# Performance work log

Hardware: AMD Instinct MI355X
Metric: run time of the kernel (lower is better)

The kernel has to match this reference:

```python
import jax, jax.numpy as jnp
import numpy as np

N, D = 8192, 128
TEMPERATURE = 0.07
EPS = 1e-8
NEG_FILL = -9e15


def setup_inputs() -> dict:
    key = jax.random.key(0)
    feats = jax.random.normal(key, (N, D), dtype=jnp.float32)
    # SimCLR-style positive-pair mask: row i's positive is row (i + N//2) % N.
    # Exactly one positive per row, as required by the original broadcast.
    label = jnp.roll(jnp.eye(N, dtype=jnp.int32), N // 2, axis=1)
    return {"feats": feats, "label": label}


def reference(feats, label):
    # F.cosine_similarity clamps each norm at eps before dividing.
    norms = jnp.linalg.norm(feats, axis=-1, keepdims=True)
    nf = feats / jnp.maximum(norms, EPS)            # [N, D] unit rows
    cos_sim = nf @ nf.T                             # [N, N] cosine similarities
    n = cos_sim.shape[0]
    self_mask = jnp.eye(n, dtype=bool)
    cos_sim = jnp.where(self_mask, NEG_FILL, cos_sim)
    cos_sim = cos_sim / TEMPERATURE
    pos_mask = (label == 1)
    # Exactly one positive per row -> masked sum == cos_sim[pos_mask] in row order.
    pos = jnp.sum(jnp.where(pos_mask, cos_sim, 0.0), axis=-1)  # [N]
    lse = jax.nn.logsumexp(cos_sim, axis=-1)                    # [N]
    return jnp.mean(-pos + lse)
```

## Files before the change

kernel.cpp:

```cpp
#include <hip/hip_runtime.h>


#define NN 8192
#define DD 128

typedef __bf16 bf16x8 __attribute__((ext_vector_type(8)));
typedef float f32x4 __attribute__((ext_vector_type(4)));
typedef unsigned int u32x4 __attribute__((ext_vector_type(4)));

constexpr float kM     = 1.0f / 0.07f;
constexpr float kScale = 1.4426950408889634f / 0.07f;
constexpr float kLn2   = 0.6931471805599453f;

__device__ inline unsigned short f2bf(float f) {
  unsigned int u = __float_as_uint(f);
  unsigned int r = (u + 0x7FFFu + ((u >> 16) & 1u)) >> 16;
  return (unsigned short)r;
}

__global__ __launch_bounds__(256) void k_normalize(const float* __restrict__ feats,
                                                   unsigned short* __restrict__ nfb) {
  int tid = threadIdx.x;
  int lane = tid & 63;
  int row = blockIdx.x * 4 + (tid >> 6);
  float2 f = *(const float2*)(feats + (size_t)row * DD + lane * 2);
  float ss = f.x * f.x + f.y * f.y;
  #pragma unroll
  for (int m = 1; m < 64; m <<= 1) ss += __shfl_xor(ss, m);
  float rn = 1.0f / fmaxf(sqrtf(ss), 1e-8f);
  unsigned int lo = f2bf(f.x * rn), hi = f2bf(f.y * rn);
  *(unsigned int*)(nfb + (size_t)row * DD + lane * 2) = lo | (hi << 16);
}

__global__ __launch_bounds__(256, 2) void k_fused(const unsigned short* __restrict__ nfb,
                                                  const int* __restrict__ label,
                                                  float* __restrict__ lpart,
                                                  int* __restrict__ pos_idx) {
  int g = blockIdx.x;
  int tid = threadIdx.x;
  int w = tid >> 6;
  int lane = tid & 63;
  int lg = lane >> 4;
  int ll = lane & 15;

  int r0 = (g >> 2) * 64;
  int cq = (g & 3) * 2048 + w * 512;
  int wid = g * 4 + w;

  const u32x4* L = (const u32x4*)label;
  int sbase = wid * 8192 + lane;

  bf16x8 afr[4][4];
  #pragma unroll
  for (int ms = 0; ms < 4; ms++) {
    const unsigned short* arow = nfb + (size_t)(r0 + ms * 16 + ll) * DD + lg * 8;
    #pragma unroll
    for (int kc = 0; kc < 4; kc++)
      afr[ms][kc] = *(const bf16x8*)(arow + kc * 32);
  }

  float lacc[4][4];
  #pragma unroll
  for (int ms = 0; ms < 4; ms++)
    #pragma unroll
    for (int r = 0; r < 4; r++) lacc[ms][r] = 0.f;

  for (int it = 0; it < 16; ++it) {
    int hcol = cq + it * 32;

    bf16x8 bfr[2][4];
    #pragma unroll
    for (int ns = 0; ns < 2; ns++) {
      const unsigned short* brow = nfb + (size_t)(hcol + ns * 16 + ll) * DD + lg * 8;
      #pragma unroll
      for (int kc = 0; kc < 4; kc++)
        bfr[ns][kc] = *(const bf16x8*)(brow + kc * 32);
    }

    u32x4 sv[8];
    #pragma unroll
    for (int j = 0; j < 8; j++)
      sv[j] = __builtin_nontemporal_load(&L[sbase + it * 512 + j * 64]);

    f32x4 acc[4][2];
    #pragma unroll
    for (int ms = 0; ms < 4; ms++)
      #pragma unroll
      for (int ns = 0; ns < 2; ns++) acc[ms][ns] = (f32x4){0.f, 0.f, 0.f, 0.f};
    #pragma unroll
    for (int kc = 0; kc < 4; kc++)
      #pragma unroll
      for (int ns = 0; ns < 2; ns++)
        #pragma unroll
        for (int ms = 0; ms < 4; ms++)
          acc[ms][ns] = __builtin_amdgcn_mfma_f32_16x16x32_bf16(afr[ms][kc], bfr[ns][kc], acc[ms][ns], 0, 0, 0);

    bool mayDiag = (hcol < r0 + 64) && (hcol + 32 > r0);
    if (mayDiag) {
      #pragma unroll
      for (int ms = 0; ms < 4; ms++) {
        int growb = r0 + ms * 16 + lg * 4;
        #pragma unroll
        for (int ns = 0; ns < 2; ns++) {
          int gcol = hcol + ns * 16 + ll;
          #pragma unroll
          for (int r = 0; r < 4; r++) {
            float s = (growb + r == gcol) ? -3.0e38f : acc[ms][ns][r];
            lacc[ms][r] += __builtin_amdgcn_exp2f((s - 1.0f) * kScale);
          }
        }
      }
    } else {
      #pragma unroll
      for (int ms = 0; ms < 4; ms++)
        #pragma unroll
        for (int ns = 0; ns < 2; ns++)
          #pragma unroll
          for (int r = 0; r < 4; r++)
            lacc[ms][r] += __builtin_amdgcn_exp2f((acc[ms][ns][r] - 1.0f) * kScale);
    }

    unsigned any = 0;
    #pragma unroll
    for (int j = 0; j < 8; j++) any |= sv[j][0] | sv[j][1] | sv[j][2] | sv[j][3];
    if (any) {
      #pragma unroll
      for (int j = 0; j < 8; j++) {
        if (sv[j][0] | sv[j][1] | sv[j][2] | sv[j][3]) {
          int gi = (sbase + it * 512 + j * 64) * 4;
          int row = gi >> 13, col = gi & (NN - 1);
          if (sv[j][0] == 1u) pos_idx[row] = col;
          if (sv[j][1] == 1u) pos_idx[row] = col + 1;
          if (sv[j][2] == 1u) pos_idx[row] = col + 2;
          if (sv[j][3] == 1u) pos_idx[row] = col + 3;
        }
      }
    }
  }

  #pragma unroll
  for (int ms = 0; ms < 4; ms++)
    #pragma unroll
    for (int r = 0; r < 4; r++) {
      float v = lacc[ms][r];
      v += __shfl_xor(v, 1); v += __shfl_xor(v, 2);
      v += __shfl_xor(v, 4); v += __shfl_xor(v, 8);
      lacc[ms][r] = v;
    }
  if (ll == 0) {
    int slot = (g & 3) * 4 + w;
    #pragma unroll
    for (int ms = 0; ms < 4; ms++)
      #pragma unroll
      for (int r = 0; r < 4; r++) {
        int grow = r0 + ms * 16 + lg * 4 + r;
        lpart[(size_t)slot * NN + grow] = lacc[ms][r];
      }
  }
}

__global__ __launch_bounds__(256) void k_finalize(const unsigned short* __restrict__ nfb,
                                                  const float* __restrict__ lpart,
                                                  const int* __restrict__ pos_idx,
                                                  float* __restrict__ bpart) {
  int i = blockIdx.x * 256 + threadIdx.x;
  float l = 0.f;
  #pragma unroll
  for (int s = 0; s < 16; s++) l += lpart[(size_t)s * NN + i];
  float lse = kM + __builtin_amdgcn_logf(l) * kLn2;
  int p = pos_idx[i] & (NN - 1);
  const u32x4* ri = (const u32x4*)(nfb + (size_t)i * DD);
  const u32x4* rp = (const u32x4*)(nfb + (size_t)p * DD);
  float dot = 0.f;
  #pragma unroll
  for (int c = 0; c < 16; c++) {
    u32x4 a = ri[c], bb = rp[c];
    #pragma unroll
    for (int e = 0; e < 4; e++) {
      float al = __uint_as_float(a[e] << 16), ah = __uint_as_float(a[e] & 0xFFFF0000u);
      float bl = __uint_as_float(bb[e] << 16), bh = __uint_as_float(bb[e] & 0xFFFF0000u);
      dot += al * bl + ah * bh;
    }
  }
  float val = lse - dot * kM;
  #pragma unroll
  for (int m = 1; m < 64; m <<= 1) val += __shfl_xor(val, m);
  __shared__ float wsum[4];
  if ((threadIdx.x & 63) == 0) wsum[threadIdx.x >> 6] = val;
  __syncthreads();
  if (threadIdx.x == 0) bpart[blockIdx.x] = wsum[0] + wsum[1] + wsum[2] + wsum[3];
}

__global__ void k_reduce(const float* __restrict__ bpart, float* __restrict__ out) {
  int t = threadIdx.x;
  float v = (t < 32) ? bpart[t] : 0.f;
  #pragma unroll
  for (int m = 1; m < 64; m <<= 1) v += __shfl_xor(v, m);
  if (t == 0) out[0] = v * (1.0f / (float)NN);
}

extern "C" void kernel_launch(void* const* d_in, const int* in_sizes, int n_in,
                              void* d_out, int out_size, void* d_ws, size_t ws_size,
                              hipStream_t stream) {
  (void)in_sizes; (void)n_in; (void)out_size; (void)ws_size;
  const float* feats = (const float*)d_in[0];
  const int* label = (const int*)d_in[1];
  float* out = (float*)d_out;

  char* ws = (char*)d_ws;
  unsigned short* nfb = (unsigned short*)ws;
  float* lpart = (float*)(ws + 2 * 1024 * 1024);
  int* pos_idx = (int*)(ws + 2 * 1024 * 1024 + 524288);
  float* bpart = (float*)(ws + 2 * 1024 * 1024 + 524288 + 32768);

  k_normalize<<<NN / 4, 256, 0, stream>>>(feats, nfb);
  k_fused<<<512, 256, 0, stream>>>(nfb, label, lpart, pos_idx);
  k_finalize<<<NN / 256, 256, 0, stream>>>(nfb, lpart, pos_idx, bpart);
  k_reduce<<<1, 64, 0, stream>>>(bpart, out);
}
```

Before: 72.47 us.

## Halve row tile per block, double grid, and fold final reduce into atomics

```diff
diff --git a/kernel.cpp b/kernel.cpp
--- a/kernel.cpp
+++ b/kernel.cpp
@@ -32,7 +32,7 @@
   *(unsigned int*)(nfb + (size_t)row * DD + lane * 2) = lo | (hi << 16);
 }
 
-__global__ __launch_bounds__(256, 2) void k_fused(const unsigned short* __restrict__ nfb,
+__global__ __launch_bounds__(256, 4) void k_fused(const unsigned short* __restrict__ nfb,
                                                   const int* __restrict__ label,
                                                   float* __restrict__ lpart,
                                                   int* __restrict__ pos_idx) {
@@ -43,27 +43,23 @@
   int lg = lane >> 4;
   int ll = lane & 15;
 
-  int r0 = (g >> 2) * 64;
+  int r0 = (g >> 2) * 32;
   int cq = (g & 3) * 2048 + w * 512;
   int wid = g * 4 + w;
 
   const u32x4* L = (const u32x4*)label;
-  int sbase = wid * 8192 + lane;
-
-  bf16x8 afr[4][4];
-  #pragma unroll
-  for (int ms = 0; ms < 4; ms++) {
+  int sbase = wid * 4096 + lane;
+
+  bf16x8 afr[2][4];
+  #pragma unroll
+  for (int ms = 0; ms < 2; ms++) {
     const unsigned short* arow = nfb + (size_t)(r0 + ms * 16 + ll) * DD + lg * 8;
     #pragma unroll
     for (int kc = 0; kc < 4; kc++)
       afr[ms][kc] = *(const bf16x8*)(arow + kc * 32);
   }
 
-  float lacc[4][4];
-  #pragma unroll
-  for (int ms = 0; ms < 4; ms++)
-    #pragma unroll
-    for (int r = 0; r < 4; r++) lacc[ms][r] = 0.f;
+  float lacc[2][4] = {{0.f, 0.f, 0.f, 0.f}, {0.f, 0.f, 0.f, 0.f}};
 
   for (int it = 0; it < 16; ++it) {
     int hcol = cq + it * 32;
@@ -77,28 +73,25 @@
         bfr[ns][kc] = *(const bf16x8*)(brow + kc * 32);
     }
 
-    u32x4 sv[8];
-    #pragma unroll
-    for (int j = 0; j < 8; j++)
-      sv[j] = __builtin_nontemporal_load(&L[sbase + it * 512 + j * 64]);
-
-    f32x4 acc[4][2];
-    #pragma unroll
-    for (int ms = 0; ms < 4; ms++)
-      #pragma unroll
-      for (int ns = 0; ns < 2; ns++) acc[ms][ns] = (f32x4){0.f, 0.f, 0.f, 0.f};
+    u32x4 sv[4];
+    #pragma unroll
+    for (int j = 0; j < 4; j++)
+      sv[j] = *(&L[sbase + it * 256 + j * 64]);
+
+    f32x4 acc[2][2] = {{{0.f,0.f,0.f,0.f},{0.f,0.f,0.f,0.f}},
+                       {{0.f,0.f,0.f,0.f},{0.f,0.f,0.f,0.f}}};
     #pragma unroll
     for (int kc = 0; kc < 4; kc++)
       #pragma unroll
       for (int ns = 0; ns < 2; ns++)
         #pragma unroll
-        for (int ms = 0; ms < 4; ms++)
+        for (int ms = 0; ms < 2; ms++)
           acc[ms][ns] = __builtin_amdgcn_mfma_f32_16x16x32_bf16(afr[ms][kc], bfr[ns][kc], acc[ms][ns], 0, 0, 0);
 
-    bool mayDiag = (hcol < r0 + 64) && (hcol + 32 > r0);
+    bool mayDiag = (hcol < r0 + 32) && (hcol + 32 > r0);
     if (mayDiag) {
       #pragma unroll
-      for (int ms = 0; ms < 4; ms++) {
+      for (int ms = 0; ms < 2; ms++) {
         int growb = r0 + ms * 16 + lg * 4;
         #pragma unroll
         for (int ns = 0; ns < 2; ns++) {
@@ -112,7 +105,7 @@
       }
     } else {
       #pragma unroll
-      for (int ms = 0; ms < 4; ms++)
+      for (int ms = 0; ms < 2; ms++)
         #pragma unroll
         for (int ns = 0; ns < 2; ns++)
           #pragma unroll
@@ -122,12 +115,12 @@
 
     unsigned any = 0;
     #pragma unroll
-    for (int j = 0; j < 8; j++) any |= sv[j][0] | sv[j][1] | sv[j][2] | sv[j][3];
+    for (int j = 0; j < 4; j++) any |= sv[j][0] | sv[j][1] | sv[j][2] | sv[j][3];
     if (any) {
       #pragma unroll
-      for (int j = 0; j < 8; j++) {
+      for (int j = 0; j < 4; j++) {
         if (sv[j][0] | sv[j][1] | sv[j][2] | sv[j][3]) {
-          int gi = (sbase + it * 512 + j * 64) * 4;
+          int gi = (sbase + it * 256 + j * 64) * 4;
           int row = gi >> 13, col = gi & (NN - 1);
           if (sv[j][0] == 1u) pos_idx[row] = col;
           if (sv[j][1] == 1u) pos_idx[row] = col + 1;
@@ -139,7 +132,7 @@
   }
 
   #pragma unroll
-  for (int ms = 0; ms < 4; ms++)
+  for (int ms = 0; ms < 2; ms++)
     #pragma unroll
     for (int r = 0; r < 4; r++) {
       float v = lacc[ms][r];
@@ -150,7 +143,7 @@
   if (ll == 0) {
     int slot = (g & 3) * 4 + w;
     #pragma unroll
-    for (int ms = 0; ms < 4; ms++)
+    for (int ms = 0; ms < 2; ms++)
       #pragma unroll
       for (int r = 0; r < 4; r++) {
         int grow = r0 + ms * 16 + lg * 4 + r;
@@ -162,7 +155,7 @@
 __global__ __launch_bounds__(256) void k_finalize(const unsigned short* __restrict__ nfb,
                                                   const float* __restrict__ lpart,
                                                   const int* __restrict__ pos_idx,
-                                                  float* __restrict__ bpart) {
+                                                  float* __restrict__ out) {
   int i = blockIdx.x * 256 + threadIdx.x;
   float l = 0.f;
   #pragma unroll
@@ -188,15 +181,8 @@
   __shared__ float wsum[4];
   if ((threadIdx.x & 63) == 0) wsum[threadIdx.x >> 6] = val;
   __syncthreads();
-  if (threadIdx.x == 0) bpart[blockIdx.x] = wsum[0] + wsum[1] + wsum[2] + wsum[3];
-}
-
-__global__ void k_reduce(const float* __restrict__ bpart, float* __restrict__ out) {
-  int t = threadIdx.x;
-  float v = (t < 32) ? bpart[t] : 0.f;
-  #pragma unroll
-  for (int m = 1; m < 64; m <<= 1) v += __shfl_xor(v, m);
-  if (t == 0) out[0] = v * (1.0f / (float)NN);
+  if (threadIdx.x == 0)
+    atomicAdd(out, (wsum[0] + wsum[1] + wsum[2] + wsum[3]) * (1.0f / (float)NN));
 }
 
 extern "C" void kernel_launch(void* const* d_in, const int* in_sizes, int n_in,
@@ -211,10 +197,9 @@
   unsigned short* nfb = (unsigned short*)ws;
   float* lpart = (float*)(ws + 2 * 1024 * 1024);
   int* pos_idx = (int*)(ws + 2 * 1024 * 1024 + 524288);
-  float* bpart = (float*)(ws + 2 * 1024 * 1024 + 524288 + 32768);
-
+
+  hipMemsetAsync(out, 0, sizeof(float), stream);
   k_normalize<<<NN / 4, 256, 0, stream>>>(feats, nfb);
-  k_fused<<<512, 256, 0, stream>>>(nfb, label, lpart, pos_idx);
-  k_finalize<<<NN / 256, 256, 0, stream>>>(nfb, lpart, pos_idx, bpart);
-  k_reduce<<<1, 64, 0, stream>>>(bpart, out);
-}
+  k_fused<<<1024, 256, 0, stream>>>(nfb, label, lpart, pos_idx);
+  k_finalize<<<NN / 256, 256, 0, stream>>>(nfb, lpart, pos_idx, out);
+}
```

After: 97.43 us. 34.4% more time.
